# Optimization experiments

Measured on AMD Instinct MI355X. Metric: run time of the kernel, lower is better.

The kernel has to match this reference:

```python
import jax, jax.numpy as jnp
import numpy as np

H, W = 256, 256
BLOCK_SIZES = [16, 1024, 1024, 24]


def get_binary_position_encoding(shape):
    # Per-pixel binary encoding of the (row, col) coordinates, MSB-first.
    encs = []
    for d in shape:
        nb = int(np.ceil(np.log2(d)))
        bits = (jnp.arange(d)[:, None] >> jnp.arange(nb - 1, -1, -1)[None, :]) & 1
        encs.append(bits.astype(bool))
    a = jnp.broadcast_to(encs[0][:, None, :], (shape[0], shape[1], encs[0].shape[-1]))
    b = jnp.broadcast_to(encs[1][None, :, :], (shape[0], shape[1], encs[1].shape[-1]))
    return jnp.concatenate([a, b], axis=-1)  # (H, W, 16) bool


def block_forward(x, mask, thr):
    # Original: expand x to (N, dim_in, dim_out), XNOR with mask, sum over dim_in,
    # threshold. XNOR-popcount == #{i : x[n,i] == mask[i,o]}, computed here as two
    # GEMMs without materializing the (N, dim_in, dim_out) intermediate.
    xf = x.astype(jnp.float32)
    mf = mask.astype(jnp.float32)
    sums = xf @ mf + (1.0 - xf) @ (1.0 - mf)  # exact integer counts in fp32
    return sums > thr.astype(jnp.float32)[None, :]


def bits_to_int(x):
    # (..., 8) bool bits, MSB-first -> int
    weights = (2 ** jnp.arange(7, -1, -1)).astype(jnp.int32)
    return jnp.sum(x.astype(jnp.int32) * weights, axis=-1)


def setup_inputs() -> dict:
    key = jax.random.key(0)
    ks = jax.random.split(key, 7)
    inp = {"image": jax.random.uniform(ks[0], (3, H, W), jnp.float32) * 255.0}
    for i, (di, do) in enumerate(zip(BLOCK_SIZES[:-1], BLOCK_SIZES[1:])):
        inp[f"mask{i}"] = jax.random.uniform(ks[1 + 2 * i], (di, do)) < 0.5
        inp[f"thr{i}"] = jax.random.randint(ks[2 + 2 * i], (do,), 0, di).astype(jnp.int32)
    return inp


def reference(image, mask0, thr0, mask1, thr1, mask2, thr2):
    pos = get_binary_position_encoding((H, W))      # (H, W, 16)
    x = pos.reshape(-1, pos.shape[-1])              # (H*W, 16) bool
    for m, t in ((mask0, thr0), (mask1, thr1), (mask2, thr2)):
        x = block_forward(x, m, t)
    x = x.reshape(H, W, 3, 8)
    x = bits_to_int(x)                              # (H, W, 3) int32
    x = jnp.transpose(x, (2, 0, 1))                 # (3, H, W)
    error = x.astype(jnp.float32) - image
    return x, error
```

## Files before the change

### kernel.cpp

```cpp
#include <hip/hip_runtime.h>
#include <stdint.h>

#define WS_CA   0
#define WS_CB   262144
#define WS_M2P  524288
#define WS_CARR 527360
#define WS_BF   532480
#define WS_X2   1581056

typedef int v4i  __attribute__((ext_vector_type(4)));
typedef int v16i __attribute__((ext_vector_type(16)));

__device__ __forceinline__ v4i expand16(unsigned h) {
  v4i a;
  a.x = (int)(__umul24(h & 15u,         0x00204081u) & 0x01010101u);
  a.y = (int)(__umul24((h >> 4) & 15u,  0x00204081u) & 0x01010101u);
  a.z = (int)(__umul24((h >> 8) & 15u,  0x00204081u) & 0x01010101u);
  a.w = (int)(__umul24((h >> 12) & 15u, 0x00204081u) & 0x01010101u);
  return a;
}

__device__ inline int detect_mode(const unsigned char* p) {
  unsigned nonalign = 0;
  for (int i = 0; i < 64; i++)
    if (i & 3) nonalign |= p[i];
  if (nonalign == 0) return 1;
  bool f32ok = true;
  for (int e = 0; e < 16; e++) {
    const unsigned char* q = p + 4 * e;
    bool one  = (q[0] == 0 && q[1] == 0 && q[2] == 0x80 && q[3] == 0x3F);
    bool zero = (q[0] == 0 && q[1] == 0 && q[2] == 0 && q[3] == 0);
    if (!(one || zero)) { f32ok = false; break; }
  }
  return f32ok ? 2 : 0;
}

__device__ inline int maskbit(const unsigned char* p, int idx, int mode) {
  if (mode == 1) return ((const int*)p)[idx] & 1;
  if (mode == 2) return ((const float*)p)[idx] != 0.0f;
  return p[idx] & 1;
}

__global__ __launch_bounds__(256) void prep_kernel(
    const unsigned char* __restrict__ mask0, const int* __restrict__ thr0,
    const unsigned char* __restrict__ mask1, const unsigned char* __restrict__ mask2,
    signed char* __restrict__ cA, unsigned char* __restrict__ cB,
    unsigned char* __restrict__ Bf, unsigned* __restrict__ M2p) {
  __shared__ int smode;
  if (threadIdx.x == 0) smode = detect_mode(mask1);
  __syncthreads();
  int mode = smode;
  int gid = blockIdx.x * 256 + threadIdx.x;
  if (gid < 524288) {
    int which = gid >> 18;
    int idx = gid & 262143;
    int hw = idx >> 10;
    int o  = idx & 1023;
    int base = which ? 8 : 0;
    int cnt = 0;
#pragma unroll
    for (int i = 0; i < 8; i++) {
      int xb = (hw >> (7 - i)) & 1;
      int mb = maskbit(mask0, (base + i) * 1024 + o, mode);
      cnt += (xb == mb);
    }
    if (which) cB[idx] = (unsigned char)cnt;
    else       cA[idx] = (signed char)(cnt - thr0[o]);
    return;
  }
  int g1 = gid - 524288;
  if (g1 < 262144) {
    int o  = g1 & 1023;
    int kk = g1 >> 10;
    unsigned u = 0;
#pragma unroll
    for (int j = 0; j < 4; j++)
      u |= (maskbit(mask1, (4 * kk + j) * 1024 + o, mode) ? 0x01u : 0xFFu) << (8 * j);
    unsigned off = ((unsigned)(o >> 5) << 15) + ((unsigned)(kk >> 3) << 10) +
                   ((unsigned)((kk >> 2) & 1) << 9) + ((unsigned)(o & 31) << 4) +
                   ((unsigned)(kk & 3) << 2);
    *reinterpret_cast<unsigned*>(Bf + off) = u;
    return;
  }
  int g2 = g1 - 262144;
  if (g2 < 768) {
    int kw = g2 / 24, o = g2 % 24;
    unsigned wv = 0;
    for (int b = 0; b < 32; b++)
      wv |= (unsigned)maskbit(mask2, (kw * 32 + b) * 24 + o, mode) << b;
    M2p[o * 32 + kw] = wv;
  }
}

__global__ __launch_bounds__(64) void popm_kernel(
    const unsigned char* __restrict__ Bf, const int* __restrict__ thr1,
    int* __restrict__ carr) {
  int o = blockIdx.x;
  int t = threadIdx.x;
  const uint4* p = reinterpret_cast<const uint4*>(
      Bf + ((unsigned)(o >> 5) << 15) + ((unsigned)(t >> 1) << 10) +
      ((unsigned)(t & 1) << 9) + ((unsigned)(o & 31) << 4));
  uint4 v = *p;
  int s = __popc(v.x) + __popc(v.y) + __popc(v.z) + __popc(v.w);
#pragma unroll
  for (int d = 32; d >= 1; d >>= 1) s += __shfl_down(s, d);
  if (t == 0) {
    int n1 = (8192 - s) / 7;
    carr[o] = thr1[o] + n1 - 1024;
  }
}

__global__ __launch_bounds__(512) void main_kernel(
    const signed char* __restrict__ cA, const unsigned char* __restrict__ cB,
    const unsigned char* __restrict__ Bf, const int* __restrict__ carr,
    unsigned* __restrict__ X2p) {
  __shared__ v4i Ae4[1024];
  __shared__ unsigned lbits[2112];
  int t = threadIdx.x;
  int lane = t & 63;
  int wv = t >> 6;
  int bid = blockIdx.x;
  int n0 = bid << 6;
  int h = n0 >> 8;
  int w0 = n0 & 255;
  int ocrot = bid & 7;
  int kqrot = (bid >> 3) & 3;

  {
    int o1 = t, o2 = t + 512;
    int av1 = (int)cA[h * 1024 + o1];
    int av2 = (int)cA[h * 1024 + o2];
    const unsigned char* cb = cB + (unsigned)w0 * 1024;
#pragma unroll 1
    for (int r4 = 0; r4 < 64; r4 += 4) {
      int v1[4], v2[4];
#pragma unroll
      for (int i = 0; i < 4; i++) {
        v1[i] = (int)cb[(unsigned)(r4 + i) * 1024 + o1];
        v2[i] = (int)cb[(unsigned)(r4 + i) * 1024 + o2];
      }
#pragma unroll
      for (int i = 0; i < 4; i++) {
        int r = r4 + i;
        unsigned long long bal1 = __ballot((av1 + v1[i]) > 0);
        unsigned long long bal2 = __ballot((av2 + v2[i]) > 0);
        if (lane == 0) {
          lbits[r * 33 + wv * 2]          = (unsigned)bal1;
          lbits[r * 33 + wv * 2 + 1]      = (unsigned)(bal1 >> 32);
          lbits[r * 33 + 16 + wv * 2]     = (unsigned)bal2;
          lbits[r * 33 + 16 + wv * 2 + 1] = (unsigned)(bal2 >> 32);
        }
      }
    }
  }

  int g = lane >> 5;
  int col = lane & 31;
  int r_ex = t & 63;
  int cl0  = (t >> 6) << 1;

#pragma unroll 1
  for (int pass = 0; pass < 2; pass++) {
    int ocp = (pass << 4) + (((wv + ocrot) & 7) << 1);
    const unsigned char* bp0 = Bf + ((unsigned)ocp << 15) + (g << 9) + (col << 4);
    const unsigned char* bp1 = bp0 + 32768;

    v16i acc00 = {0,0,0,0,0,0,0,0,0,0,0,0,0,0,0,0};
    v16i acc10 = acc00, acc01 = acc00, acc11 = acc00;

#pragma unroll 1
    for (int kq = 0; kq < 4; kq++) {
      int kqe = (kq + kqrot) & 3;
      __syncthreads();
#pragma unroll
      for (int ci = 0; ci < 2; ci++) {
        int cl = cl0 + ci;
        unsigned word = lbits[r_ex * 33 + (kqe << 3) + (cl >> 1)];
        unsigned hwv = (cl & 1) ? (word >> 16) : (word & 0xFFFFu);
        Ae4[cl * 64 + r_ex] = expand16(hwv);
      }
      __syncthreads();

      int ksb = kqe << 3;
      v4i b0n = *reinterpret_cast<const v4i*>(bp0 + (ksb) * 1024);
      v4i b1n = *reinterpret_cast<const v4i*>(bp1 + (ksb) * 1024);
#pragma unroll 1
      for (int ksl = 0; ksl < 8; ksl++) {
        v4i b0 = b0n, b1 = b1n;
        if (ksl < 7) {
          b0n = *reinterpret_cast<const v4i*>(bp0 + (ksb + ksl + 1) * 1024);
          b1n = *reinterpret_cast<const v4i*>(bp1 + (ksb + ksl + 1) * 1024);
        }
        int c = 2 * ksl + g;
        v4i a0 = Ae4[c * 64 + col];
        v4i a1 = Ae4[c * 64 + 32 + col];
        acc00 = __builtin_amdgcn_mfma_i32_32x32x32_i8(a0, b0, acc00, 0, 0, 0);
        acc10 = __builtin_amdgcn_mfma_i32_32x32x32_i8(a1, b0, acc10, 0, 0, 0);
        acc01 = __builtin_amdgcn_mfma_i32_32x32x32_i8(a0, b1, acc01, 0, 0, 0);
        acc11 = __builtin_amdgcn_mfma_i32_32x32x32_i8(a1, b1, acc11, 0, 0, 0);
      }
    }

#pragma unroll
    for (int s = 0; s < 2; s++) {
      int oc = ocp + s;
      int cv = carr[(oc << 5) + col];
#pragma unroll
      for (int rt = 0; rt < 2; rt++) {
        v16i av = (s == 0) ? (rt == 0 ? acc00 : acc10)
                           : (rt == 0 ? acc01 : acc11);
#pragma unroll
        for (int reg = 0; reg < 16; reg++) {
          int px_lo = (rt << 5) + (reg & 3) + ((reg >> 2) << 3);
          bool bit = av[reg] > cv;
          unsigned long long bal = __ballot(bit);
          if (lane == 0) {
            X2p[(unsigned)(n0 + px_lo) * 32 + oc]     = (unsigned)bal;
            X2p[(unsigned)(n0 + px_lo + 4) * 32 + oc] = (unsigned)(bal >> 32);
          }
        }
      }
    }
  }
}

__global__ __launch_bounds__(256) void l2_kernel(
    const uint4* __restrict__ X2p4, const unsigned* __restrict__ M2p,
    const int* __restrict__ thr2, const float* __restrict__ image,
    float* __restrict__ out) {
  __shared__ unsigned lm2[768];
  int t = threadIdx.x;
  for (int r = t; r < 768; r += 256) lm2[r] = M2p[r];
  __syncthreads();
  int n = blockIdx.x * 256 + t;
  uint4 xw[8];
#pragma unroll
  for (int q = 0; q < 8; q++) xw[q] = X2p4[(unsigned)n * 8 + q];
#pragma unroll
  for (int c = 0; c < 3; c++) {
    int val = 0;
#pragma unroll
    for (int b = 0; b < 8; b++) {
      int o = c * 8 + b;
      const unsigned* m = &lm2[o * 32];
      unsigned acc2 = 0;
#pragma unroll
      for (int q = 0; q < 8; q++) {
        acc2 += __popc(xw[q].x ^ m[q * 4 + 0]);
        acc2 += __popc(xw[q].y ^ m[q * 4 + 1]);
        acc2 += __popc(xw[q].z ^ m[q * 4 + 2]);
        acc2 += __popc(xw[q].w ^ m[q * 4 + 3]);
      }
      int bit = ((int)(1024u - acc2)) > thr2[o];
      val |= bit << (7 - b);
    }
    out[c * 65536 + n] = (float)val;
    out[196608 + c * 65536 + n] = (float)val - image[c * 65536 + n];
  }
}

extern "C" void kernel_launch(void* const* d_in, const int* in_sizes, int n_in,
                              void* d_out, int out_size, void* d_ws, size_t ws_size,
                              hipStream_t stream) {
  const float*         image = (const float*)d_in[0];
  const unsigned char* mask0 = (const unsigned char*)d_in[1];
  const int*           thr0  = (const int*)d_in[2];
  const unsigned char* mask1 = (const unsigned char*)d_in[3];
  const int*           thr1  = (const int*)d_in[4];
  const unsigned char* mask2 = (const unsigned char*)d_in[5];
  const int*           thr2  = (const int*)d_in[6];
  char* ws = (char*)d_ws;
  signed char*    cA    = (signed char*)(ws + WS_CA);
  unsigned char*  cB    = (unsigned char*)(ws + WS_CB);
  unsigned*       M2p   = (unsigned*)(ws + WS_M2P);
  int*            carr  = (int*)(ws + WS_CARR);
  unsigned char*  Bf    = (unsigned char*)(ws + WS_BF);
  unsigned*       X2p   = (unsigned*)(ws + WS_X2);
  float* out = (float*)d_out;

  hipLaunchKernelGGL(prep_kernel, dim3(3075), dim3(256), 0, stream,
                     mask0, thr0, mask1, mask2, cA, cB, Bf, M2p);
  hipLaunchKernelGGL(popm_kernel, dim3(1024), dim3(64), 0, stream,
                     Bf, thr1, carr);
  hipLaunchKernelGGL(main_kernel, dim3(1024), dim3(512), 0, stream,
                     cA, cB, Bf, carr, X2p);
  hipLaunchKernelGGL(l2_kernel, dim3(256), dim3(256), 0, stream,
                     (const uint4*)X2p, M2p, thr2, image, out);
}
```

Baseline: 120.7 us.

## Shrink per-wave output tile to one column block with four passes

```diff
diff --git a/kernel.cpp b/kernel.cpp
--- a/kernel.cpp
+++ b/kernel.cpp
@@ -160,13 +160,12 @@
   int cl0  = (t >> 6) << 1;
 
 #pragma unroll 1
-  for (int pass = 0; pass < 2; pass++) {
-    int ocp = (pass << 4) + (((wv + ocrot) & 7) << 1);
-    const unsigned char* bp0 = Bf + ((unsigned)ocp << 15) + (g << 9) + (col << 4);
-    const unsigned char* bp1 = bp0 + 32768;
-
-    v16i acc00 = {0,0,0,0,0,0,0,0,0,0,0,0,0,0,0,0};
-    v16i acc10 = acc00, acc01 = acc00, acc11 = acc00;
+  for (int pass = 0; pass < 4; pass++) {
+    int oc = (pass << 3) | ((wv + ocrot) & 7);
+    const unsigned char* bp = Bf + ((unsigned)oc << 15) + (g << 9) + (col << 4);
+
+    v16i acc0 = {0,0,0,0,0,0,0,0,0,0,0,0,0,0,0,0};
+    v16i acc1 = acc0;
 
 #pragma unroll 1
     for (int kq = 0; kq < 4; kq++) {
@@ -182,42 +181,32 @@
       __syncthreads();
 
       int ksb = kqe << 3;
-      v4i b0n = *reinterpret_cast<const v4i*>(bp0 + (ksb) * 1024);
-      v4i b1n = *reinterpret_cast<const v4i*>(bp1 + (ksb) * 1024);
+      v4i bn = *reinterpret_cast<const v4i*>(bp + (ksb) * 1024);
 #pragma unroll 1
       for (int ksl = 0; ksl < 8; ksl++) {
-        v4i b0 = b0n, b1 = b1n;
-        if (ksl < 7) {
-          b0n = *reinterpret_cast<const v4i*>(bp0 + (ksb + ksl + 1) * 1024);
-          b1n = *reinterpret_cast<const v4i*>(bp1 + (ksb + ksl + 1) * 1024);
-        }
+        v4i b = bn;
+        if (ksl < 7)
+          bn = *reinterpret_cast<const v4i*>(bp + (ksb + ksl + 1) * 1024);
         int c = 2 * ksl + g;
         v4i a0 = Ae4[c * 64 + col];
         v4i a1 = Ae4[c * 64 + 32 + col];
-        acc00 = __builtin_amdgcn_mfma_i32_32x32x32_i8(a0, b0, acc00, 0, 0, 0);
-        acc10 = __builtin_amdgcn_mfma_i32_32x32x32_i8(a1, b0, acc10, 0, 0, 0);
-        acc01 = __builtin_amdgcn_mfma_i32_32x32x32_i8(a0, b1, acc01, 0, 0, 0);
-        acc11 = __builtin_amdgcn_mfma_i32_32x32x32_i8(a1, b1, acc11, 0, 0, 0);
-      }
-    }
-
-#pragma unroll
-    for (int s = 0; s < 2; s++) {
-      int oc = ocp + s;
-      int cv = carr[(oc << 5) + col];
-#pragma unroll
-      for (int rt = 0; rt < 2; rt++) {
-        v16i av = (s == 0) ? (rt == 0 ? acc00 : acc10)
-                           : (rt == 0 ? acc01 : acc11);
-#pragma unroll
-        for (int reg = 0; reg < 16; reg++) {
-          int px_lo = (rt << 5) + (reg & 3) + ((reg >> 2) << 3);
-          bool bit = av[reg] > cv;
-          unsigned long long bal = __ballot(bit);
-          if (lane == 0) {
-            X2p[(unsigned)(n0 + px_lo) * 32 + oc]     = (unsigned)bal;
-            X2p[(unsigned)(n0 + px_lo + 4) * 32 + oc] = (unsigned)(bal >> 32);
-          }
+        acc0 = __builtin_amdgcn_mfma_i32_32x32x32_i8(a0, b, acc0, 0, 0, 0);
+        acc1 = __builtin_amdgcn_mfma_i32_32x32x32_i8(a1, b, acc1, 0, 0, 0);
+      }
+    }
+
+    int cv = carr[(oc << 5) + col];
+#pragma unroll
+    for (int rt = 0; rt < 2; rt++) {
+      v16i av = (rt == 0) ? acc0 : acc1;
+#pragma unroll
+      for (int reg = 0; reg < 16; reg++) {
+        int px_lo = (rt << 5) + (reg & 3) + ((reg >> 2) << 3);
+        bool bit = av[reg] > cv;
+        unsigned long long bal = __ballot(bit);
+        if (lane == 0) {
+          X2p[(unsigned)(n0 + px_lo) * 32 + oc]     = (unsigned)bal;
+          X2p[(unsigned)(n0 + px_lo + 4) * 32 + oc] = (unsigned)(bal >> 32);
         }
       }
     }
```

Result: slower. 127.0 us (+5.2%).

## Fuse final binary layer into main kernel via shared-memory bit buffer

Applied to the files above, without the earlier changes.

```diff
diff --git a/kernel.cpp b/kernel.cpp
--- a/kernel.cpp
+++ b/kernel.cpp
@@ -6,7 +6,6 @@
 #define WS_M2P  524288
 #define WS_CARR 527360
 #define WS_BF   532480
-#define WS_X2   1581056
 
 typedef int v4i  __attribute__((ext_vector_type(4)));
 typedef int v16i __attribute__((ext_vector_type(16)));
@@ -113,9 +112,12 @@
 __global__ __launch_bounds__(512) void main_kernel(
     const signed char* __restrict__ cA, const unsigned char* __restrict__ cB,
     const unsigned char* __restrict__ Bf, const int* __restrict__ carr,
-    unsigned* __restrict__ X2p) {
+    const unsigned* __restrict__ M2p, const int* __restrict__ thr2,
+    const float* __restrict__ image, float* __restrict__ out) {
   __shared__ v4i Ae4[1024];
   __shared__ unsigned lbits[2112];
+  __shared__ unsigned xbits[2112];
+  __shared__ unsigned lm2[768];
   int t = threadIdx.x;
   int lane = t & 63;
   int wv = t >> 6;
@@ -126,6 +128,8 @@
   int ocrot = bid & 7;
   int kqrot = (bid >> 3) & 3;
 
+  for (int r = t; r < 768; r += 512) lm2[r] = M2p[r];
+
   {
     int o1 = t, o2 = t + 512;
     int av1 = (int)cA[h * 1024 + o1];
@@ -215,47 +219,36 @@
           bool bit = av[reg] > cv;
           unsigned long long bal = __ballot(bit);
           if (lane == 0) {
-            X2p[(unsigned)(n0 + px_lo) * 32 + oc]     = (unsigned)bal;
-            X2p[(unsigned)(n0 + px_lo + 4) * 32 + oc] = (unsigned)(bal >> 32);
+            xbits[px_lo * 33 + oc]       = (unsigned)bal;
+            xbits[(px_lo + 4) * 33 + oc] = (unsigned)(bal >> 32);
           }
         }
       }
     }
   }
-}
-
-__global__ __launch_bounds__(256) void l2_kernel(
-    const uint4* __restrict__ X2p4, const unsigned* __restrict__ M2p,
-    const int* __restrict__ thr2, const float* __restrict__ image,
-    float* __restrict__ out) {
-  __shared__ unsigned lm2[768];
-  int t = threadIdx.x;
-  for (int r = t; r < 768; r += 256) lm2[r] = M2p[r];
   __syncthreads();
-  int n = blockIdx.x * 256 + t;
-  uint4 xw[8];
-#pragma unroll
-  for (int q = 0; q < 8; q++) xw[q] = X2p4[(unsigned)n * 8 + q];
-#pragma unroll
-  for (int c = 0; c < 3; c++) {
-    int val = 0;
-#pragma unroll
-    for (int b = 0; b < 8; b++) {
-      int o = c * 8 + b;
-      const unsigned* m = &lm2[o * 32];
-      unsigned acc2 = 0;
-#pragma unroll
-      for (int q = 0; q < 8; q++) {
-        acc2 += __popc(xw[q].x ^ m[q * 4 + 0]);
-        acc2 += __popc(xw[q].y ^ m[q * 4 + 1]);
-        acc2 += __popc(xw[q].z ^ m[q * 4 + 2]);
-        acc2 += __popc(xw[q].w ^ m[q * 4 + 3]);
-      }
-      int bit = ((int)(1024u - acc2)) > thr2[o];
-      val |= bit << (7 - b);
-    }
-    out[c * 65536 + n] = (float)val;
-    out[196608 + c * 65536 + n] = (float)val - image[c * 65536 + n];
+
+  if (t < 256) {
+    int px = t >> 2, sub = t & 3;
+    if (sub < 3) {
+      int c = sub;
+      int n = n0 + px;
+      int val = 0;
+#pragma unroll
+      for (int b = 0; b < 8; b++) {
+        int o = c * 8 + b;
+        unsigned acc2s = 0;
+#pragma unroll
+        for (int wi = 0; wi < 32; wi++) {
+          int w = (wi + px) & 31;
+          acc2s += __popc(xbits[px * 33 + w] ^ lm2[o * 32 + w]);
+        }
+        int bit = ((int)(1024u - acc2s)) > thr2[o];
+        val |= bit << (7 - b);
+      }
+      out[c * 65536 + n] = (float)val;
+      out[196608 + c * 65536 + n] = (float)val - image[c * 65536 + n];
+    }
   }
 }
 
@@ -275,7 +268,6 @@
   unsigned*       M2p   = (unsigned*)(ws + WS_M2P);
   int*            carr  = (int*)(ws + WS_CARR);
   unsigned char*  Bf    = (unsigned char*)(ws + WS_BF);
-  unsigned*       X2p   = (unsigned*)(ws + WS_X2);
   float* out = (float*)d_out;
 
   hipLaunchKernelGGL(prep_kernel, dim3(3075), dim3(256), 0, stream,
@@ -283,7 +275,5 @@
   hipLaunchKernelGGL(popm_kernel, dim3(1024), dim3(64), 0, stream,
                      Bf, thr1, carr);
   hipLaunchKernelGGL(main_kernel, dim3(1024), dim3(512), 0, stream,
-                     cA, cB, Bf, carr, X2p);
-  hipLaunchKernelGGL(l2_kernel, dim3(256), dim3(256), 0, stream,
-                     (const uint4*)X2p, M2p, thr2, image, out);
-}
+                     cA, cB, Bf, carr, M2p, thr2, image, out);
+}
```

Result: slower. 133.3 us (+10.4%).
